# Optimization experiments

Measured on AMD Instinct MI355X. Metric: run time of the kernel, lower is better.

Reference implementation:

```python
import jax, jax.numpy as jnp
import numpy as np

RANK = 16
ALPHA = 32
SCALING = ALPHA / RANK  # alpha / rank


def setup_inputs() -> dict:
    key = jax.random.key(0)
    k_x, k_w, k_b, k_a, k_bb = jax.random.split(key, 5)
    B, S, D_IN, D_OUT = 4, 2048, 4096, 4096
    x = jax.random.normal(k_x, (B, S, D_IN), dtype=jnp.float32)
    W = jax.random.normal(k_w, (D_OUT, D_IN), dtype=jnp.float32) * (1.0 / np.sqrt(D_IN))
    b = jax.random.normal(k_b, (D_OUT,), dtype=jnp.float32) * 0.02
    # LoRA init: A ~ N(0, 2/rank); B is zeros in the module, but we use small
    # random values so the adapter path is numerically exercised.
    lora_A = jax.random.normal(k_a, (RANK, D_IN), dtype=jnp.float32) * np.sqrt(2.0 / RANK)
    lora_B = jax.random.normal(k_bb, (D_OUT, RANK), dtype=jnp.float32) * 0.02
    return {"x": x, "W": W, "b": b, "lora_A": lora_A, "lora_B": lora_B}


def reference(x, W, b, lora_A, lora_B):
    # Base linear: x @ W^T + b
    base = jnp.einsum("bsd,od->bso", x, W) + b
    # LoRA path, fused as two rank-r matmuls (never materializing B@A):
    # (x @ A^T) @ B^T * scaling  ==  F.linear(x, B@A) * scaling
    xa = jnp.einsum("bsd,rd->bsr", x, lora_A)      # [B,S,r]
    lora = jnp.einsum("bsr,or->bso", xa, lora_B)    # [B,S,D_out]
    return base + lora * SCALING
```

## Files before the change

### kernel.cpp

```cpp
#include <hip/hip_runtime.h>
#include <hip/hip_bf16.h>

#define K_DIM 4096
#define N_DIM 4096
#define R_DIM 16
#define SCALING_F 2.0f

#define BM 256
#define BN 256
#define BK 64

typedef __attribute__((ext_vector_type(8))) short bf16x8;
typedef __attribute__((ext_vector_type(4))) float f32x4;

__device__ __forceinline__ ushort f2bf(float f) {
  union { float f; unsigned u; } v; v.f = f;
  unsigned u = v.u;
  u += 0x7FFF + ((u >> 16) & 1);
  return (ushort)(u >> 16);
}

__global__ __launch_bounds__(256) void prepass_kernel(
    const float* __restrict__ x, ushort* __restrict__ xb,
    const float* __restrict__ W, const float* __restrict__ A,
    const float* __restrict__ Bl, ushort* __restrict__ wb, long n4) {
  if (blockIdx.x < N_DIM) {
    int o = blockIdx.x;
    float breg[R_DIM];
#pragma unroll
    for (int r = 0; r < R_DIM; ++r) breg[r] = Bl[o * R_DIM + r] * SCALING_F;
    for (int d0 = threadIdx.x * 4; d0 < K_DIM; d0 += blockDim.x * 4) {
      float4 w = *(const float4*)(W + (size_t)o * K_DIM + d0);
      float a0 = w.x, a1 = w.y, a2 = w.z, a3 = w.w;
#pragma unroll
      for (int r = 0; r < R_DIM; ++r) {
        float4 a = *(const float4*)(A + (size_t)r * K_DIM + d0);
        a0 += breg[r] * a.x; a1 += breg[r] * a.y;
        a2 += breg[r] * a.z; a3 += breg[r] * a.w;
      }
      ushort4 ob;
      ob.x = f2bf(a0); ob.y = f2bf(a1); ob.z = f2bf(a2); ob.w = f2bf(a3);
      *(ushort4*)(wb + (size_t)o * K_DIM + d0) = ob;
    }
  } else {
    long i = (long)(blockIdx.x - N_DIM) * blockDim.x + threadIdx.x;
    long stride = 2048L * blockDim.x;
    for (; i < n4; i += stride) {
      long idx = i * 4;
      float4 v = *(const float4*)(x + idx);
      ushort4 o;
      o.x = f2bf(v.x); o.y = f2bf(v.y); o.z = f2bf(v.z); o.w = f2bf(v.w);
      *(ushort4*)(xb + idx) = o;
    }
  }
}


#define RS 8192L

#define GLOAD(SRC, LOFF)                                                    \
  __builtin_amdgcn_global_load_lds(                                         \
      (const __attribute__((address_space(1))) void*)(SRC),                 \
      (__attribute__((address_space(3))) void*)(smem + (LOFF)), 16, 0, 0)

#define LDSA(BUF) ((BUF) * 32768)
#define LDSB(BUF) (65536 + (BUF) * 32768)

#define ST_A_EVEN(T, BUF) do {                                              \
    GLOAD(aS + (size_t)(T) * 128,            LDSA(BUF) + ldsDst);           \
    GLOAD(aS + (size_t)(T) * 128 + 128 * RS, LDSA(BUF) + 16384 + ldsDst); } while (0)
#define ST_A_ODD(T, BUF) do {                                               \
    GLOAD(aS + (size_t)(T) * 128 + 64 * RS,  LDSA(BUF) + 8192 + ldsDst);    \
    GLOAD(aS + (size_t)(T) * 128 + 192 * RS, LDSA(BUF) + 24576 + ldsDst); } while (0)
#define ST_B_H0(T, BUF) do {                                                \
    GLOAD(bS + (size_t)(T) * 128,            LDSB(BUF) + ldsDst);           \
    GLOAD(bS + (size_t)(T) * 128 + 64 * RS,  LDSB(BUF) + 8192 + ldsDst); } while (0)
#define ST_B_H1(T, BUF) do {                                                \
    GLOAD(bS + (size_t)(T) * 128 + 128 * RS, LDSB(BUF) + 16384 + ldsDst);   \
    GLOAD(bS + (size_t)(T) * 128 + 192 * RS, LDSB(BUF) + 24576 + ldsDst); } while (0)

#define LDA(M, CK, BUF) (*(const bf16x8*)(smem + LDSA(BUF) + aRd + (M) * 2048 + (CK)))
#define LDB(N, CK, BUF) (*(const bf16x8*)(smem + LDSB(BUF) + bRd + (N) * 2048 + (CK)))

#define MFMA16(MB, KK) do {                                                 \
    _Pragma("unroll") for (int mm = 0; mm < 4; ++mm)                        \
      _Pragma("unroll") for (int nn = 0; nn < 4; ++nn)                      \
        acc[(MB) + mm][nn] = __builtin_amdgcn_mfma_f32_16x16x32_bf16(       \
            afr[mm], bfr[nn][KK], acc[(MB) + mm][nn], 0, 0, 0); } while (0)

#define PH_EXEC(MB, KK) do {                                                \
    __builtin_amdgcn_s_barrier();                                           \
    asm volatile("s_waitcnt lgkmcnt(0)");                                   \
    __builtin_amdgcn_s_setprio(1);                                          \
    MFMA16(MB, KK);                                                         \
    __builtin_amdgcn_s_setprio(0);                                          \
    __builtin_amdgcn_s_barrier(); } while (0)

__global__ __launch_bounds__(512, 2) void gemm_lora_kernel(
    const ushort* __restrict__ Ab, const ushort* __restrict__ Bb,
    const float* __restrict__ bias, float* __restrict__ C) {
  __shared__ char smem[131072];

  const int tid = threadIdx.x;
  const int wave = tid >> 6, lane = tid & 63;
  const int wm = wave >> 2, wn = wave & 3;
  const int fr = lane & 15, fq = lane >> 4;

  const int bid = blockIdx.x;
  const int bm = ((bid & 7) << 2) + ((bid >> 3) & 3);
  const int bn = bid >> 5;

  const int trow = tid >> 3;
  const int tswz = ((tid & 7) << 4) ^ ((trow & 7) << 4);
  const char* aS = (const char*)Ab + (size_t)(bm * BM + trow) * RS + tswz;
  const char* bS = (const char*)Bb + (size_t)(bn * BN + trow) * RS + tswz;
  const int ldsDst = tid << 4;

  const int sa  = (fr & 7) << 4;
  const int cK0 = (fq << 4) ^ sa;
  const int cK1 = (64 | (fq << 4)) ^ sa;
  const int aRd = ((wm << 7) + fr) << 7;
  const int bRd = ((wn << 6) + fr) << 7;

  f32x4 acc[8][4];
#pragma unroll
  for (int m = 0; m < 8; ++m)
#pragma unroll
    for (int n = 0; n < 4; ++n) acc[m][n] = (f32x4){0.f, 0.f, 0.f, 0.f};
  bf16x8 afr[4], bfr[4][2];

  ST_B_H0(0, 0); ST_B_H1(0, 0); ST_A_EVEN(0, 0); ST_A_ODD(0, 0);
  ST_B_H0(1, 1); ST_B_H1(1, 1); ST_A_EVEN(1, 1);
  asm volatile("s_waitcnt vmcnt(6)" ::: "memory");
  __builtin_amdgcn_s_barrier();

  const int NIT = K_DIM / (2 * BK);
#pragma unroll 1
  for (int i = 0; i < NIT; ++i) {
    const int t1 = 2 * i + 1, t2 = 2 * i + 2, t3 = 2 * i + 3;
    const bool last = (i == NIT - 1);

#pragma unroll
    for (int n = 0; n < 4; ++n) { bfr[n][0] = LDB(n, cK0, 0); bfr[n][1] = LDB(n, cK1, 0); }
#pragma unroll
    for (int m = 0; m < 4; ++m) afr[m] = LDA(m, cK0, 0);
    ST_A_ODD(t1, 1);
    asm volatile("s_waitcnt lgkmcnt(8)");
    PH_EXEC(0, 0);

#pragma unroll
    for (int m = 0; m < 4; ++m) afr[m] = LDA(m, cK1, 0);
    if (!last) ST_B_H0(t2, 0);
    PH_EXEC(0, 1);

#pragma unroll
    for (int m = 0; m < 4; ++m) afr[m] = LDA(m + 4, cK0, 0);
    if (!last) ST_B_H1(t2, 0);
    PH_EXEC(4, 0);

#pragma unroll
    for (int m = 0; m < 4; ++m) afr[m] = LDA(m + 4, cK1, 0);
    if (!last) ST_A_EVEN(t2, 0);
    __builtin_amdgcn_s_barrier();
    asm volatile("s_waitcnt lgkmcnt(0)");
    __builtin_amdgcn_s_setprio(1);
    MFMA16(4, 1);
    __builtin_amdgcn_s_setprio(0);
    if (last) asm volatile("s_waitcnt vmcnt(0)" ::: "memory");
    else      asm volatile("s_waitcnt vmcnt(6)" ::: "memory");
    __builtin_amdgcn_s_barrier();

#pragma unroll
    for (int n = 0; n < 4; ++n) { bfr[n][0] = LDB(n, cK0, 1); bfr[n][1] = LDB(n, cK1, 1); }
#pragma unroll
    for (int m = 0; m < 4; ++m) afr[m] = LDA(m, cK0, 1);
    if (!last) ST_A_ODD(t2, 0);
    asm volatile("s_waitcnt lgkmcnt(8)");
    PH_EXEC(0, 0);

#pragma unroll
    for (int m = 0; m < 4; ++m) afr[m] = LDA(m, cK1, 1);
    if (!last) ST_B_H0(t3, 1);
    PH_EXEC(0, 1);

#pragma unroll
    for (int m = 0; m < 4; ++m) afr[m] = LDA(m + 4, cK0, 1);
    if (!last) ST_B_H1(t3, 1);
    PH_EXEC(4, 0);

#pragma unroll
    for (int m = 0; m < 4; ++m) afr[m] = LDA(m + 4, cK1, 1);
    if (!last) ST_A_EVEN(t3, 1);
    __builtin_amdgcn_s_barrier();
    asm volatile("s_waitcnt lgkmcnt(0)");
    __builtin_amdgcn_s_setprio(1);
    MFMA16(4, 1);
    __builtin_amdgcn_s_setprio(0);
    if (!last) {
      asm volatile("s_waitcnt vmcnt(6)" ::: "memory");
      __builtin_amdgcn_s_barrier();
    }
  }

  const int ccol0 = bn * BN + wn * 64 + fr;
  float bv[4];
#pragma unroll
  for (int n = 0; n < 4; ++n) bv[n] = bias[ccol0 + n * 16];
  const int crow0 = bm * BM + wm * 128 + fq * 4;
#pragma unroll
  for (int m = 0; m < 8; ++m)
#pragma unroll
    for (int n = 0; n < 4; ++n)
#pragma unroll
      for (int v = 0; v < 4; ++v) {
        int row = crow0 + m * 16 + v;
        C[(size_t)row * N_DIM + ccol0 + n * 16] = acc[m][n][v] + bv[n];
      }
}

extern "C" void kernel_launch(void* const* d_in, const int* in_sizes, int n_in,
                              void* d_out, int out_size, void* d_ws, size_t ws_size,
                              hipStream_t stream) {
  const float* x  = (const float*)d_in[0];
  const float* W  = (const float*)d_in[1];
  const float* b  = (const float*)d_in[2];
  const float* lA = (const float*)d_in[3];
  const float* lB = (const float*)d_in[4];
  float* out = (float*)d_out;

  const int M = in_sizes[0] / K_DIM;

  ushort* xb = (ushort*)d_ws;
  ushort* wb = xb + (size_t)M * K_DIM;

  long n4 = (long)M * K_DIM / 4;
  prepass_kernel<<<N_DIM + 2048, 256, 0, stream>>>(x, xb, W, lA, lB, wb, n4);
  gemm_lora_kernel<<<(M / BM) * (N_DIM / BN), 512, 0, stream>>>(xb, wb, b, out);
}
```

Before: 315.5 us.

## Software-pipeline LDS fragment loads behind MFMA phases in LoRA GEMM

```diff
diff --git a/kernel.cpp b/kernel.cpp
--- a/kernel.cpp
+++ b/kernel.cpp
@@ -82,19 +82,27 @@
 #define LDA(M, CK, BUF) (*(const bf16x8*)(smem + LDSA(BUF) + aRd + (M) * 2048 + (CK)))
 #define LDB(N, CK, BUF) (*(const bf16x8*)(smem + LDSB(BUF) + bRd + (N) * 2048 + (CK)))
 
+#define PF_A(MB, CK, BUF) do {                                              \
+    afr[0] = LDA((MB) + 0, CK, BUF); afr[1] = LDA((MB) + 1, CK, BUF);       \
+    afr[2] = LDA((MB) + 2, CK, BUF); afr[3] = LDA((MB) + 3, CK, BUF); } while (0)
+#define PF_B_ALL(BUF) do {                                                  \
+    bfr[0][0] = LDB(0, cK0, BUF); bfr[0][1] = LDB(0, cK1, BUF);             \
+    bfr[1][0] = LDB(1, cK0, BUF); bfr[1][1] = LDB(1, cK1, BUF);             \
+    bfr[2][0] = LDB(2, cK0, BUF); bfr[2][1] = LDB(2, cK1, BUF);             \
+    bfr[3][0] = LDB(3, cK0, BUF); bfr[3][1] = LDB(3, cK1, BUF); } while (0)
+
 #define MFMA16(MB, KK) do {                                                 \
     _Pragma("unroll") for (int mm = 0; mm < 4; ++mm)                        \
       _Pragma("unroll") for (int nn = 0; nn < 4; ++nn)                      \
         acc[(MB) + mm][nn] = __builtin_amdgcn_mfma_f32_16x16x32_bf16(       \
             afr[mm], bfr[nn][KK], acc[(MB) + mm][nn], 0, 0, 0); } while (0)
 
-#define PH_EXEC(MB, KK) do {                                                \
+#define PH_CORE(MB, KK) do {                                                \
     __builtin_amdgcn_s_barrier();                                           \
     asm volatile("s_waitcnt lgkmcnt(0)");                                   \
     __builtin_amdgcn_s_setprio(1);                                          \
     MFMA16(MB, KK);                                                         \
-    __builtin_amdgcn_s_setprio(0);                                          \
-    __builtin_amdgcn_s_barrier(); } while (0)
+    __builtin_amdgcn_s_setprio(0); } while (0)
 
 __global__ __launch_bounds__(512, 2) void gemm_lora_kernel(
     const ushort* __restrict__ Ab, const ushort* __restrict__ Bb,
@@ -133,6 +141,8 @@
   ST_B_H0(1, 1); ST_B_H1(1, 1); ST_A_EVEN(1, 1);
   asm volatile("s_waitcnt vmcnt(6)" ::: "memory");
   __builtin_amdgcn_s_barrier();
+  PF_B_ALL(0);
+  PF_A(0, cK0, 0);
 
   const int NIT = K_DIM / (2 * BK);
 #pragma unroll 1
@@ -140,64 +150,50 @@
     const int t1 = 2 * i + 1, t2 = 2 * i + 2, t3 = 2 * i + 3;
     const bool last = (i == NIT - 1);
 
-#pragma unroll
-    for (int n = 0; n < 4; ++n) { bfr[n][0] = LDB(n, cK0, 0); bfr[n][1] = LDB(n, cK1, 0); }
-#pragma unroll
-    for (int m = 0; m < 4; ++m) afr[m] = LDA(m, cK0, 0);
     ST_A_ODD(t1, 1);
-    asm volatile("s_waitcnt lgkmcnt(8)");
-    PH_EXEC(0, 0);
-
-#pragma unroll
-    for (int m = 0; m < 4; ++m) afr[m] = LDA(m, cK1, 0);
+    PH_CORE(0, 0);
+    PF_A(0, cK1, 0);
+    __builtin_amdgcn_s_barrier();
+
     if (!last) ST_B_H0(t2, 0);
-    PH_EXEC(0, 1);
-
-#pragma unroll
-    for (int m = 0; m < 4; ++m) afr[m] = LDA(m + 4, cK0, 0);
+    PH_CORE(0, 1);
+    PF_A(4, cK0, 0);
+    __builtin_amdgcn_s_barrier();
+
     if (!last) ST_B_H1(t2, 0);
-    PH_EXEC(4, 0);
-
-#pragma unroll
-    for (int m = 0; m < 4; ++m) afr[m] = LDA(m + 4, cK1, 0);
+    PH_CORE(4, 0);
+    PF_A(4, cK1, 0);
+    if (last) asm volatile("s_waitcnt vmcnt(0)" ::: "memory");
+    else      asm volatile("s_waitcnt vmcnt(4)" ::: "memory");
+    __builtin_amdgcn_s_barrier();
+
     if (!last) ST_A_EVEN(t2, 0);
-    __builtin_amdgcn_s_barrier();
-    asm volatile("s_waitcnt lgkmcnt(0)");
-    __builtin_amdgcn_s_setprio(1);
-    MFMA16(4, 1);
-    __builtin_amdgcn_s_setprio(0);
-    if (last) asm volatile("s_waitcnt vmcnt(0)" ::: "memory");
-    else      asm volatile("s_waitcnt vmcnt(6)" ::: "memory");
-    __builtin_amdgcn_s_barrier();
-
-#pragma unroll
-    for (int n = 0; n < 4; ++n) { bfr[n][0] = LDB(n, cK0, 1); bfr[n][1] = LDB(n, cK1, 1); }
-#pragma unroll
-    for (int m = 0; m < 4; ++m) afr[m] = LDA(m, cK0, 1);
+    PH_CORE(4, 1);
+    PF_B_ALL(1);
+    PF_A(0, cK0, 1);
+    __builtin_amdgcn_s_barrier();
+
     if (!last) ST_A_ODD(t2, 0);
-    asm volatile("s_waitcnt lgkmcnt(8)");
-    PH_EXEC(0, 0);
-
-#pragma unroll
-    for (int m = 0; m < 4; ++m) afr[m] = LDA(m, cK1, 1);
+    PH_CORE(0, 0);
+    PF_A(0, cK1, 1);
+    __builtin_amdgcn_s_barrier();
+
     if (!last) ST_B_H0(t3, 1);
-    PH_EXEC(0, 1);
-
-#pragma unroll
-    for (int m = 0; m < 4; ++m) afr[m] = LDA(m + 4, cK0, 1);
+    PH_CORE(0, 1);
+    PF_A(4, cK0, 1);
+    __builtin_amdgcn_s_barrier();
+
     if (!last) ST_B_H1(t3, 1);
-    PH_EXEC(4, 0);
-
-#pragma unroll
-    for (int m = 0; m < 4; ++m) afr[m] = LDA(m + 4, cK1, 1);
+    PH_CORE(4, 0);
+    PF_A(4, cK1, 1);
+    if (!last) asm volatile("s_waitcnt vmcnt(4)" ::: "memory");
+    __builtin_amdgcn_s_barrier();
+
     if (!last) ST_A_EVEN(t3, 1);
-    __builtin_amdgcn_s_barrier();
-    asm volatile("s_waitcnt lgkmcnt(0)");
-    __builtin_amdgcn_s_setprio(1);
-    MFMA16(4, 1);
-    __builtin_amdgcn_s_setprio(0);
+    PH_CORE(4, 1);
     if (!last) {
-      asm volatile("s_waitcnt vmcnt(6)" ::: "memory");
+      PF_B_ALL(0);
+      PF_A(0, cK0, 0);
       __builtin_amdgcn_s_barrier();
     }
   }
```

Result: no change. 312.0 us (-1.1%).
